# Kernel tuning notes

Hardware: AMD Instinct MI355X
Metric: run time of the kernel (lower is better)

## Reference

```python
import jax, jax.numpy as jnp
from jax import lax
import numpy as np

GC_LAMBDA = 0.75
N = 8388608  # chain length (number of graph nodes between source and sink)


def setup_inputs() -> dict:
    key = jax.random.key(0)
    inputs = jax.random.uniform(key, (N,), dtype=jnp.float32)  # probabilities in [0,1)
    return {"inputs": inputs}


def reference(inputs):
    # Min s-t cut of the chain graph == Viterbi DP over binary labels x_i:
    #   E(x) = sum_i [x_i==1 ? (1-p_i) : p_i] + lam * sum_{i>0} [x_i != x_{i-1}]
    # Label 1 <=> node on source side (reachable set) in the min cut.
    lam = jnp.float32(GC_LAMBDA)
    cost0 = inputs          # x_i = 0: cut source->i edge, capacity p_i
    cost1 = 1.0 - inputs    # x_i = 1: cut i->sink edge, capacity 1 - p_i

    def fwd(carry, costs):
        a0, a1 = carry       # best energy ending in state 0 / 1 (renormalized)
        c0, c1 = costs
        from1 = a1 + lam < a0   # best predecessor of current state 0 is state 1
        from0 = a0 + lam < a1   # best predecessor of current state 1 is state 0
        n0 = c0 + jnp.minimum(a0, a1 + lam)
        n1 = c1 + jnp.minimum(a1, a0 + lam)
        m = jnp.minimum(n0, n1)  # keep carries small for fp32 accuracy over long chains
        return (n0 - m, n1 - m), (from1, from0)

    (a0, a1), (from1, from0) = lax.scan(
        fwd, (cost0[0], cost1[0]), (cost0[1:], cost1[1:])
    )
    last = a1 < a0  # label of the final node (True -> 1)

    def bwd(state, chs):
        f1, f0 = chs
        prev = jnp.where(state, ~f0, f1)  # backtrack the argmin pointers
        return prev, prev

    _, states = lax.scan(bwd, last, (from1, from0), reverse=True)
    labels = jnp.concatenate([states, last[None]])  # [N] bool
    return labels.astype(jnp.int32)
```

## Files before the change

kernel.cpp:

```cpp
#include <hip/hip_runtime.h>
#include <stdint.h>


#define LAM 0.75f
constexpr int N_TOTAL = 8388608;
constexpr int SEG = 32;
constexpr int NSEG = N_TOTAL / SEG;
constexpr int NBLK_AB = NSEG / 256;
constexpr int NWORD = N_TOTAL / 64;
constexpr int NBLK_FILL = NWORD / 256;

__device__ __forceinline__ float dstep(float d, float p) {
    float e0 = fminf(fmaxf(d, 0.0f), LAM);
    float e1 = fminf(fmaxf(-d, 0.0f), LAM);
    return (p + e0) - ((1.0f - p) + e1);
}

__device__ float seg0_end(const float* __restrict__ p) {
    float p0 = p[0];
    float a0 = p0, a1 = 1.0f - p0;
    float t0 = fminf(a0, a1 + LAM);
    float t1 = fminf(a1, a0 + LAM);
    float p1 = p[1];
    float d = (p1 + t0) - ((1.0f - p1) + t1);
    for (int i = 2; i < SEG; ++i) d = dstep(d, p[i]);
    return d;
}

union SegU { float4 q[8]; float f[32]; };

__global__ __launch_bounds__(256, 4) void k_ab(const float* __restrict__ p,
        uint2* __restrict__ evsg) {
    __shared__ float s_dh[256];
    __shared__ uint8_t s_ok[256];
    const int t = threadIdx.x;
    const int s = blockIdx.x * 256 + t;

    SegU u;
    const float4* g4 = (const float4*)(p + (size_t)s * SEG);
    #pragma unroll
    for (int i = 0; i < 8; ++i) u.q[i] = g4[i];

    float dh = 2.0f, dl = -2.0f;
    #pragma unroll
    for (int i = 0; i < SEG; ++i) {
        float pi = u.f[i];
        dh = dstep(dh, pi);
        dl = dstep(dl, pi);
    }
    s_dh[t] = dh;
    s_ok[t] = (dh == dl) ? 1 : 0;
    __syncthreads();

    float d = 0.0f;
    uint32_t em = 0, gm = 0;
    if (s == 0) {
        float p0 = u.f[0];
        float a0 = p0, a1 = 1.0f - p0;
        bool f1 = (a1 + LAM) < a0;
        bool f0 = (a0 + LAM) < a1;
        em |= (uint32_t)(f1 || f0); gm |= (uint32_t)f1;
        float t0 = fminf(a0, a1 + LAM);
        float t1 = fminf(a1, a0 + LAM);
        float p1 = u.f[1];
        d = (p1 + t0) - ((1.0f - p1) + t1);
        em |= (uint32_t)(fabsf(d) > LAM) << 1;
        gm |= (uint32_t)(d > LAM) << 1;
        #pragma unroll
        for (int i = 2; i < SEG; ++i) {
            d = dstep(d, u.f[i]);
            em |= (uint32_t)(fabsf(d) > LAM) << i;
            gm |= (uint32_t)(d > LAM) << i;
        }
    } else {
        int back = t - 1;
        while (back >= 0 && !s_ok[back]) --back;
        int startSeg;
        if (back >= 0) {
            d = s_dh[back];
            startSeg = blockIdx.x * 256 + back;
        } else {
            int v = blockIdx.x * 256 - 1;
            for (;;) {
                if (v == 0) { d = seg0_end(p); startSeg = 0; break; }
                const float4* gv = (const float4*)(p + (size_t)v * SEG);
                float h = 2.0f, l = -2.0f;
                for (int i = 0; i < 8; ++i) {
                    float4 q = gv[i];
                    h = dstep(h, q.x); l = dstep(l, q.x);
                    h = dstep(h, q.y); l = dstep(l, q.y);
                    h = dstep(h, q.z); l = dstep(l, q.z);
                    h = dstep(h, q.w); l = dstep(l, q.w);
                }
                if (h == l) { d = h; startSeg = v; break; }
                --v;
            }
        }
        for (int v = startSeg + 1; v < s; ++v) {
            const float* sv = p + (size_t)v * SEG;
            for (int i = 0; i < SEG; ++i) d = dstep(d, sv[i]);
        }
        #pragma unroll
        for (int i = 0; i < SEG; ++i) {
            d = dstep(d, u.f[i]);
            em |= (uint32_t)(fabsf(d) > LAM) << i;
            gm |= (uint32_t)(d > LAM) << i;
        }
    }
    if (s == NSEG - 1) {
        em |= 0x80000000u;
        gm = (d > 0.0f) ? (gm | 0x80000000u) : (gm & 0x7FFFFFFFu);
    }
    evsg[s] = make_uint2(em, gm);
}

__global__ __launch_bounds__(256, 4) void k_fill(const uint4* __restrict__ evsg2,
        int* __restrict__ out) {
    __shared__ uint64_t lev[256];
    __shared__ uint64_t lsg[256];
    __shared__ int lC[256];
    const int t = threadIdx.x;
    const int b = blockIdx.x;
    const int w = b * 256 + t;

    uint4 wv = evsg2[w];
    uint64_t e = ((uint64_t)wv.z << 32) | wv.x;
    uint64_t g = ((uint64_t)wv.w << 32) | wv.y;
    lev[t] = e; lsg[t] = g;
    __syncthreads();

    int cur = 0; bool found = false;
    for (int v = t + 1; v < 256; ++v) {
        uint64_t evv = lev[v];
        if (evv) { cur = (int)((lsg[v] >> __builtin_ctzll(evv)) & 1ull); found = true; break; }
    }
    if (!found && b + 1 < NBLK_FILL) {
        int v = (b + 1) * 256;
        while (v < NWORD) {
            uint4 sv = evsg2[v];
            uint64_t evv = ((uint64_t)sv.z << 32) | sv.x;
            if (evv) {
                uint64_t sgv = ((uint64_t)sv.w << 32) | sv.y;
                cur = (int)((sgv >> __builtin_ctzll(evv)) & 1ull);
                break;
            }
            ++v;
        }
    }
    lC[t] = cur;
    __syncthreads();

    int4* o4 = (int4*)out + (size_t)b * 4096;
    #pragma unroll
    for (int i = 0; i < 16; ++i) {
        int c = i * 256 + t;
        int wl = c >> 4;
        int bb = (c & 15) * 4;
        uint64_t we = lev[wl], wg = lsg[wl];
        int wc = lC[wl];
        int4 r;
        uint64_t m = we >> (bb + 0);
        r.x = m ? (int)((wg >> (bb + 0 + __builtin_ctzll(m))) & 1ull) : wc;
        m = we >> (bb + 1);
        r.y = m ? (int)((wg >> (bb + 1 + __builtin_ctzll(m))) & 1ull) : wc;
        m = we >> (bb + 2);
        r.z = m ? (int)((wg >> (bb + 2 + __builtin_ctzll(m))) & 1ull) : wc;
        m = we >> (bb + 3);
        r.w = m ? (int)((wg >> (bb + 3 + __builtin_ctzll(m))) & 1ull) : wc;
        o4[c] = r;
    }
}

extern "C" void kernel_launch(void* const* d_in, const int* in_sizes, int n_in,
                              void* d_out, int out_size, void* d_ws, size_t ws_size,
                              hipStream_t stream) {
    (void)in_sizes; (void)n_in; (void)out_size; (void)ws_size;
    const float* p = (const float*)d_in[0];
    int* out = (int*)d_out;
    uint2* evsg = (uint2*)d_ws;

    k_ab<<<dim3(NBLK_AB), dim3(256), 0, stream>>>(p, evsg);
    k_fill<<<dim3(NBLK_FILL), dim3(256), 0, stream>>>((const uint4*)evsg, out);
}
```

Measured before the change: 87.15 us.

## Fuse label fill into forward kernel with per-block summaries and tail fixup

Merges the event-mask kernel and the fill kernel so each block writes its output labels directly from shared memory, avoiding the workspace round trip of event/sign masks. Each block records a summary (first event sign) and the position of its last event. A small fixup kernel then rewrites the tail of each block after its last event, using the next block's summary. This removes one full pass of global traffic but adds a second, mostly redundant write of tail elements and a serial per-thread fixup loop.

```diff
diff --git a/kernel.cpp b/kernel.cpp
--- a/kernel.cpp
+++ b/kernel.cpp
@@ -6,9 +6,7 @@
 constexpr int N_TOTAL = 8388608;
 constexpr int SEG = 32;
 constexpr int NSEG = N_TOTAL / SEG;
-constexpr int NBLK_AB = NSEG / 256;
-constexpr int NWORD = N_TOTAL / 64;
-constexpr int NBLK_FILL = NWORD / 256;
+constexpr int NBLK = NSEG / 256;
 
 __device__ __forceinline__ float dstep(float d, float p) {
     float e0 = fminf(fmaxf(d, 0.0f), LAM);
@@ -29,12 +27,17 @@
 
 union SegU { float4 q[8]; float f[32]; };
 
-__global__ __launch_bounds__(256, 4) void k_ab(const float* __restrict__ p,
-        uint2* __restrict__ evsg) {
+__global__ __launch_bounds__(256, 4) void k_main(const float* __restrict__ p,
+        uint32_t* __restrict__ bsum, int* __restrict__ blast,
+        int* __restrict__ out) {
     __shared__ float s_dh[256];
     __shared__ uint8_t s_ok[256];
+    __shared__ uint32_t lev[256];
+    __shared__ uint32_t lsg[256];
+    __shared__ int lC[256];
     const int t = threadIdx.x;
-    const int s = blockIdx.x * 256 + t;
+    const int b = blockIdx.x;
+    const int s = b * 256 + t;
 
     SegU u;
     const float4* g4 = (const float4*)(p + (size_t)s * SEG);
@@ -78,9 +81,9 @@
         int startSeg;
         if (back >= 0) {
             d = s_dh[back];
-            startSeg = blockIdx.x * 256 + back;
+            startSeg = b * 256 + back;
         } else {
-            int v = blockIdx.x * 256 - 1;
+            int v = b * 256 - 1;
             for (;;) {
                 if (v == 0) { d = seg0_end(p); startSeg = 0; break; }
                 const float4* gv = (const float4*)(p + (size_t)v * SEG);
@@ -111,64 +114,70 @@
         em |= 0x80000000u;
         gm = (d > 0.0f) ? (gm | 0x80000000u) : (gm & 0x7FFFFFFFu);
     }
-    evsg[s] = make_uint2(em, gm);
+    lev[t] = em;
+    lsg[t] = gm;
+    __syncthreads();
+
+    {
+        int cur = 0;
+        for (int v = t + 1; v < 256; ++v) {
+            uint32_t evv = lev[v];
+            if (evv) { cur = (int)((lsg[v] >> __builtin_ctz(evv)) & 1u); break; }
+        }
+        lC[t] = cur;
+    }
+    if (t == 0) {
+        uint32_t summ = 0;
+        for (int v = 0; v < 256; ++v) {
+            uint32_t evv = lev[v];
+            if (evv) { summ = 2u | (uint32_t)((lsg[v] >> __builtin_ctz(evv)) & 1u); break; }
+        }
+        bsum[b] = summ;
+    }
+    if (t == 1) {
+        int lp = -1;
+        for (int v = 255; v >= 0; --v) {
+            uint32_t evv = lev[v];
+            if (evv) { lp = b * 8192 + v * 32 + (31 - __builtin_clz(evv)); break; }
+        }
+        blast[b] = lp;
+    }
+    __syncthreads();
+
+    int4* o4 = (int4*)out + (size_t)b * 2048;
+    #pragma unroll
+    for (int i = 0; i < 8; ++i) {
+        int c = i * 256 + t;
+        int wl = c >> 3;
+        int bb = (c & 7) * 4;
+        uint32_t we = lev[wl], wg = lsg[wl];
+        int wc = lC[wl];
+        int4 r;
+        uint32_t m = we >> (bb + 0);
+        r.x = m ? (int)((wg >> (bb + 0 + __builtin_ctz(m))) & 1u) : wc;
+        m = we >> (bb + 1);
+        r.y = m ? (int)((wg >> (bb + 1 + __builtin_ctz(m))) & 1u) : wc;
+        m = we >> (bb + 2);
+        r.z = m ? (int)((wg >> (bb + 2 + __builtin_ctz(m))) & 1u) : wc;
+        m = we >> (bb + 3);
+        r.w = m ? (int)((wg >> (bb + 3 + __builtin_ctz(m))) & 1u) : wc;
+        o4[c] = r;
+    }
 }
 
-__global__ __launch_bounds__(256, 4) void k_fill(const uint4* __restrict__ evsg2,
-        int* __restrict__ out) {
-    __shared__ uint64_t lev[256];
-    __shared__ uint64_t lsg[256];
-    __shared__ int lC[256];
-    const int t = threadIdx.x;
-    const int b = blockIdx.x;
-    const int w = b * 256 + t;
-
-    uint4 wv = evsg2[w];
-    uint64_t e = ((uint64_t)wv.z << 32) | wv.x;
-    uint64_t g = ((uint64_t)wv.w << 32) | wv.y;
-    lev[t] = e; lsg[t] = g;
-    __syncthreads();
-
-    int cur = 0; bool found = false;
-    for (int v = t + 1; v < 256; ++v) {
-        uint64_t evv = lev[v];
-        if (evv) { cur = (int)((lsg[v] >> __builtin_ctzll(evv)) & 1ull); found = true; break; }
+__global__ __launch_bounds__(256) void k_fixup(const uint32_t* __restrict__ bsum,
+        const int* __restrict__ blast, int* __restrict__ out) {
+    int b = blockIdx.x * 256 + threadIdx.x;
+    int lp = blast[b];
+    int start = (lp >= 0) ? (lp + 1) : (b * 8192);
+    int end = (b + 1) * 8192;
+    if (start >= end) return;
+    int c = 0;
+    for (int v = b + 1; v < NBLK; ++v) {
+        uint32_t sv = bsum[v];
+        if (sv & 2u) { c = (int)(sv & 1u); break; }
     }
-    if (!found && b + 1 < NBLK_FILL) {
-        int v = (b + 1) * 256;
-        while (v < NWORD) {
-            uint4 sv = evsg2[v];
-            uint64_t evv = ((uint64_t)sv.z << 32) | sv.x;
-            if (evv) {
-                uint64_t sgv = ((uint64_t)sv.w << 32) | sv.y;
-                cur = (int)((sgv >> __builtin_ctzll(evv)) & 1ull);
-                break;
-            }
-            ++v;
-        }
-    }
-    lC[t] = cur;
-    __syncthreads();
-
-    int4* o4 = (int4*)out + (size_t)b * 4096;
-    #pragma unroll
-    for (int i = 0; i < 16; ++i) {
-        int c = i * 256 + t;
-        int wl = c >> 4;
-        int bb = (c & 15) * 4;
-        uint64_t we = lev[wl], wg = lsg[wl];
-        int wc = lC[wl];
-        int4 r;
-        uint64_t m = we >> (bb + 0);
-        r.x = m ? (int)((wg >> (bb + 0 + __builtin_ctzll(m))) & 1ull) : wc;
-        m = we >> (bb + 1);
-        r.y = m ? (int)((wg >> (bb + 1 + __builtin_ctzll(m))) & 1ull) : wc;
-        m = we >> (bb + 2);
-        r.z = m ? (int)((wg >> (bb + 2 + __builtin_ctzll(m))) & 1ull) : wc;
-        m = we >> (bb + 3);
-        r.w = m ? (int)((wg >> (bb + 3 + __builtin_ctzll(m))) & 1ull) : wc;
-        o4[c] = r;
-    }
+    for (int i = start; i < end; ++i) out[i] = c;
 }
 
 extern "C" void kernel_launch(void* const* d_in, const int* in_sizes, int n_in,
@@ -177,8 +186,10 @@
     (void)in_sizes; (void)n_in; (void)out_size; (void)ws_size;
     const float* p = (const float*)d_in[0];
     int* out = (int*)d_out;
-    uint2* evsg = (uint2*)d_ws;
+    char* ws = (char*)d_ws;
+    uint32_t* bsum = (uint32_t*)ws;
+    int*      blast = (int*)(ws + (size_t)NBLK * 4);
 
-    k_ab<<<dim3(NBLK_AB), dim3(256), 0, stream>>>(p, evsg);
-    k_fill<<<dim3(NBLK_FILL), dim3(256), 0, stream>>>((const uint4*)evsg, out);
+    k_main<<<dim3(NBLK), dim3(256), 0, stream>>>(p, bsum, blast, out);
+    k_fixup<<<dim3(NBLK / 256), dim3(256), 0, stream>>>(bsum, blast, out);
 }
```

Result: no change. 87.48 us (+0.4%).
